# Performance work log

Hardware: AMD Instinct MI355X
Metric: run time of the kernel (lower is better)

Reference implementation:

```python
import jax, jax.numpy as jnp
import numpy as np

E = 16      # num experts
K = 2       # top-k
EPS = np.finfo(float).eps


def setup_inputs() -> dict:
    key = jax.random.key(0)
    k1, k2, k3 = jax.random.split(key, 3)
    B, D_IN, D_OUT = 16384, 1024, 512
    x = jax.random.normal(k1, (B, D_IN), dtype=jnp.float32)
    w_router = jax.random.normal(k2, (D_IN, E), dtype=jnp.float32) * 0.02
    w_experts = jax.random.normal(k3, (E, D_IN, D_OUT), dtype=jnp.float32) * 0.02
    return {"x": x, "w_router": w_router, "w_experts": w_experts}


def reference(x, w_router, w_experts):
    # --- noisy_top_k_gating (eval path: clean logits, no noise) ---
    logits = x @ w_router                      # [B, E]
    top_vals, top_idx = jax.lax.top_k(logits, K)   # [B, K]
    top_gates = jax.nn.softmax(top_vals, axis=1)   # softmax over top-k logits
    B = x.shape[0]
    gates = jnp.zeros_like(logits).at[jnp.arange(B)[:, None], top_idx].set(top_gates)  # [B, E]

    # --- per-expert encode (dense form; zero gates null out non-dispatched pairs,
    #     matching SparseDispatcher's sparse dispatch/combine math exactly) ---
    expert_out = jnp.einsum('bd,edh->beh', x, w_experts)  # [B, E, d_out]

    # --- SparseDispatcher.combine: exp -> gate-weight -> index_add -> eps clamp -> log ---
    combined = jnp.einsum('be,beh->bh', gates, jnp.exp(expert_out))  # [B, d_out]
    combined = jnp.where(combined == 0, jnp.asarray(EPS, combined.dtype), combined)
    return jnp.log(combined)
```

## Files before the change

### kernel.cpp

```cpp
#include <hip/hip_runtime.h>
#include <hip/hip_bf16.h>
#include <stdint.h>

typedef unsigned short u16_t;
typedef unsigned int   u32_t;

#define B_ROWS  16384
#define D_IN    1024
#define D_OUT   512
#define NEXP    16
#define CNT_STRIDE 16
#define EPSF    2.2204460492503131e-16f

using short8  = __attribute__((ext_vector_type(8))) short;
using floatx4 = __attribute__((ext_vector_type(4))) float;

__device__ __forceinline__ u16_t f2bf(float f) {
    u32_t u = __float_as_uint(f);
    u += 0x7fffu + ((u >> 16) & 1u);
    return (u16_t)(u >> 16);
}

__device__ __forceinline__ void gload_lds16(const void* g, void* l) {
    __builtin_amdgcn_global_load_lds(
        (const __attribute__((address_space(1))) void*)g,
        (__attribute__((address_space(3))) void*)l, 16, 0, 0);
}

__global__ __launch_bounds__(256) void prep_kernel(
        const float* __restrict__ wr, float* __restrict__ wrT,
        const float* __restrict__ we, u16_t* __restrict__ wT,
        int* __restrict__ counts) {
    int b = blockIdx.x, t = threadIdx.x;
    if (b < 64) {
        int i = b * 256 + t;
        int e = i >> 10, d = i & 1023;
        wrT[i] = wr[d * NEXP + e];
    } else if (b == 64) {
        counts[t] = 0;
    } else {
        int bb = b - 65;
        int e  = bb >> 8;
        int k0 = ((bb >> 1) & 127) * 8;
        int n  = (bb & 1) * 256 + t;
        const float* src = we + ((size_t)e * D_IN + k0) * D_OUT + n;
        union { u16_t us[8]; uint4 v; } p;
        #pragma unroll
        for (int j = 0; j < 8; ++j) p.us[j] = f2bf(src[(size_t)j * D_OUT]);
        *(uint4*)(wT + ((size_t)e * D_OUT + n) * D_IN + k0) = p.v;
    }
}

__global__ __launch_bounds__(256) void router_kernel(
        const float* __restrict__ x, const float* __restrict__ wrT,
        int* __restrict__ counts, int* __restrict__ rowlist,
        float* __restrict__ gatelist, u16_t* __restrict__ xb) {
    __shared__ float wsh[NEXP * D_IN];
    __shared__ int hist[NEXP], base[NEXP], hist2[NEXP];
    __shared__ unsigned char eidx_sh[32][2];
    __shared__ float g_sh[32][2];

    int t = threadIdx.x;
    {
        const float4* src = (const float4*)wrT;
        float4* dst = (float4*)wsh;
        #pragma unroll
        for (int i = 0; i < 16; ++i) dst[t + 256 * i] = src[t + 256 * i];
    }
    if (t < NEXP) { hist[t] = 0; hist2[t] = 0; }
    __syncthreads();

    int lr = t >> 3, c = t & 7;
    int row = blockIdx.x * 32 + lr;
    const float4* xr = (const float4*)(x + (size_t)row * D_IN);

    double acc[NEXP];
    #pragma unroll
    for (int e = 0; e < NEXP; ++e) acc[e] = 0.0;

    for (int i = 0; i < 32; ++i) {
        int f4 = i * 8 + c;
        float4 xv = xr[f4];
        int d = f4 * 4;
        if (xb) {
            uint2 pk;
            pk.x = (u32_t)f2bf(xv.x) | ((u32_t)f2bf(xv.y) << 16);
            pk.y = (u32_t)f2bf(xv.z) | ((u32_t)f2bf(xv.w) << 16);
            *(uint2*)(xb + (size_t)row * D_IN + d) = pk;
        }
        double x0 = xv.x, x1 = xv.y, x2 = xv.z, x3 = xv.w;
        #pragma unroll
        for (int e = 0; e < NEXP; ++e) {
            float4 wv = *(const float4*)(&wsh[e * D_IN + d]);
            acc[e] += x0 * (double)wv.x;
            acc[e] += x1 * (double)wv.y;
            acc[e] += x2 * (double)wv.z;
            acc[e] += x3 * (double)wv.w;
        }
    }
    #pragma unroll
    for (int e = 0; e < NEXP; ++e) {
        acc[e] += __shfl_xor(acc[e], 1);
        acc[e] += __shfl_xor(acc[e], 2);
        acc[e] += __shfl_xor(acc[e], 4);
    }
    if (c == 0) {
        int i1 = 0; double v1 = acc[0];
        #pragma unroll
        for (int e = 1; e < NEXP; ++e) if (acc[e] > v1) { v1 = acc[e]; i1 = e; }
        int i2 = -1; double v2 = -1.0e300;
        #pragma unroll
        for (int e = 0; e < NEXP; ++e) if (e != i1 && acc[e] > v2) { v2 = acc[e]; i2 = e; }
        double ed = exp(v2 - v1);
        double s = 1.0 + ed;
        eidx_sh[lr][0] = (unsigned char)i1; g_sh[lr][0] = (float)(1.0 / s);
        eidx_sh[lr][1] = (unsigned char)i2; g_sh[lr][1] = (float)(ed / s);
        atomicAdd(&hist[i1], 1);
        atomicAdd(&hist[i2], 1);
    }
    __syncthreads();
    if (t < NEXP) base[t] = atomicAdd(&counts[t * CNT_STRIDE], hist[t]);
    __syncthreads();
    if (t < 64) {
        int r = t >> 1, sl = t & 1;
        int e = eidx_sh[r][sl];
        int pos = base[e] + atomicAdd(&hist2[e], 1);
        rowlist[e * B_ROWS + pos] = ((blockIdx.x * 32 + r) << 1) | sl;
        gatelist[e * B_ROWS + pos] = g_sh[r][sl];
    }
}

template<bool USE_CONTRIB>
__global__ __launch_bounds__(256) void moe_gemm_bf16(
        const u16_t* __restrict__ xb, const u16_t* __restrict__ wT,
        const int* __restrict__ counts, const int* __restrict__ rowlist,
        const float* __restrict__ gatelist,
        float* __restrict__ out, float* __restrict__ contrib) {
    int bid = blockIdx.x;
    int s   = bid >> 3;
    int e   = ((bid & 7) << 1) | (s >> 9);
    s &= 511;
    int tx = s & 3, ty = s >> 2;
    int n_e = counts[e * CNT_STRIDE];
    if (ty * 128 >= n_e) return;
    int n0 = tx * 128;

    __shared__ u16_t Ash[128 * 64];
    __shared__ u16_t Bsh[128 * 64];
    __shared__ int   rid_sh[128];
    __shared__ float gt_sh[128];

    int t = threadIdx.x;
    if (t < 128) {
        int gi = ty * 128 + t;
        int v = 0; float g = 0.f;
        if (gi < n_e) { v = rowlist[e * B_ROWS + gi]; g = gatelist[e * B_ROWS + gi]; }
        rid_sh[t] = v; gt_sh[t] = g;
    }
    __syncthreads();

    int lane = t & 63, wv = t >> 6;

    const u16_t* asrc[4];
    const u16_t* bsrc[4];
    #pragma unroll
    for (int r = 0; r < 4; ++r) {
        int i   = r * 256 + wv * 64 + lane;
        int row = i >> 3;
        int ss  = (i & 7) ^ (row & 7);
        asrc[r] = xb + (size_t)(rid_sh[row] >> 1) * D_IN + ss * 8;
        bsrc[r] = wT + ((size_t)e * D_OUT + n0 + row) * D_IN + ss * 8;
    }

    int wm = wv >> 1, wn = wv & 1;
    int lm = lane & 15, q = lane >> 4;
    int l7 = lm & 7;

    floatx4 acc[4][4];
    #pragma unroll
    for (int mi = 0; mi < 4; ++mi)
        #pragma unroll
        for (int ni = 0; ni < 4; ++ni)
            acc[mi][ni] = (floatx4){0.f, 0.f, 0.f, 0.f};

    for (int it = 0; it < D_IN / 64; ++it) {
        if (it) __syncthreads();
        #pragma unroll
        for (int r = 0; r < 4; ++r) {
            gload_lds16(asrc[r], (char*)Ash + r * 4096 + wv * 1024);
            gload_lds16(bsrc[r], (char*)Bsh + r * 4096 + wv * 1024);
            asrc[r] += 64; bsrc[r] += 64;
        }
        __syncthreads();

        #pragma unroll
        for (int kk = 0; kk < 2; ++kk) {
            int sw = ((((kk << 2) | q) ^ l7) << 3);
            short8 afr[4], bfr[4];
            #pragma unroll
            for (int f = 0; f < 4; ++f) {
                afr[f] = *(const short8*)(Ash + ((wm * 64 + f * 16 + lm) << 6) + sw);
                bfr[f] = *(const short8*)(Bsh + ((wn * 64 + f * 16 + lm) << 6) + sw);
            }
            #pragma unroll
            for (int mi = 0; mi < 4; ++mi)
                #pragma unroll
                for (int ni = 0; ni < 4; ++ni)
                    acc[mi][ni] = __builtin_amdgcn_mfma_f32_16x16x32_bf16(
                        afr[mi], bfr[ni], acc[mi][ni], 0, 0, 0);
        }
    }

    #pragma unroll
    for (int mi = 0; mi < 4; ++mi) {
        int rbase = wm * 64 + mi * 16 + q * 4;
        #pragma unroll
        for (int r = 0; r < 4; ++r) {
            int row = rbase + r;
            int gi = ty * 128 + row;
            bool ok = gi < n_e;
            int v = rid_sh[row];
            float g = gt_sh[row];
            size_t orow = (size_t)(v >> 1) * D_OUT;
            #pragma unroll
            for (int ni = 0; ni < 4; ++ni) {
                int c = n0 + wn * 64 + ni * 16 + lm;
                float val = g * __expf(acc[mi][ni][r]);
                if (ok) {
                    if (USE_CONTRIB) {
                        float* dst = (v & 1) ? contrib : out;
                        dst[orow + c] = val;
                    } else {
                        atomicAdd(&out[orow + c], val);
                    }
                }
            }
        }
    }
}

template<bool USE_CONTRIB>
__global__ __launch_bounds__(256) void moe_gemm(
        const float* __restrict__ x, const float* __restrict__ w,
        const int* __restrict__ counts, const int* __restrict__ rowlist,
        const float* __restrict__ gatelist,
        float* __restrict__ out, float* __restrict__ contrib) {
    int e = blockIdx.z;
    int n_e = counts[e * CNT_STRIDE];
    int ty = blockIdx.y;
    if (ty * 128 >= n_e) return;
    int n0 = blockIdx.x * 128;

    __shared__ u16_t Ash[128][40];
    __shared__ u32_t Bsh[16][132];
    __shared__ int   rid_sh[128];
    __shared__ float gt_sh[128];

    int t = threadIdx.x;
    if (t < 128) {
        int gi = ty * 128 + t;
        int v = 0; float g = 0.f;
        if (gi < n_e) { v = rowlist[e * B_ROWS + gi]; g = gatelist[e * B_ROWS + gi]; }
        rid_sh[t] = v; gt_sh[t] = g;
    }
    __syncthreads();

    int ar = t >> 1, ah = t & 1;
    const float* xptr = x + (size_t)(rid_sh[ar] >> 1) * D_IN + ah * 16;
    int bkp = t >> 4, bng = t & 15;
    const float* wptr = w + (size_t)e * (D_IN * D_OUT)
                          + (size_t)(2 * bkp) * D_OUT + n0 + bng * 8;

    int lane = t & 63, wv = t >> 6;
    int wm = wv >> 1, wn = wv & 1;
    int lm = lane & 15, q = lane >> 4;

    floatx4 acc[4][4];
    #pragma unroll
    for (int mi = 0; mi < 4; ++mi)
        #pragma unroll
        for (int ni = 0; ni < 4; ++ni)
            acc[mi][ni] = (floatx4){0.f, 0.f, 0.f, 0.f};

    for (int it = 0; it < D_IN / 32; ++it) {
        float4 av0 = *(const float4*)(xptr + 0);
        float4 av1 = *(const float4*)(xptr + 4);
        float4 av2 = *(const float4*)(xptr + 8);
        float4 av3 = *(const float4*)(xptr + 12);
        xptr += 32;
        float4 b0 = *(const float4*)(wptr + 0);
        float4 b1 = *(const float4*)(wptr + 4);
        float4 b2 = *(const float4*)(wptr + D_OUT);
        float4 b3 = *(const float4*)(wptr + D_OUT + 4);
        wptr += 32 * D_OUT;

        __syncthreads();
        {
            union { u16_t us[16]; uint4 v[2]; } ap;
            float af[16] = {av0.x, av0.y, av0.z, av0.w, av1.x, av1.y, av1.z, av1.w,
                            av2.x, av2.y, av2.z, av2.w, av3.x, av3.y, av3.z, av3.w};
            #pragma unroll
            for (int j = 0; j < 16; ++j) ap.us[j] = f2bf(af[j]);
            *(uint4*)(&Ash[ar][ah * 16])     = ap.v[0];
            *(uint4*)(&Ash[ar][ah * 16 + 8]) = ap.v[1];
        }
        {
            union { u32_t up[8]; uint4 v[2]; } bp;
            bp.up[0] = (u32_t)f2bf(b0.x) | ((u32_t)f2bf(b2.x) << 16);
            bp.up[1] = (u32_t)f2bf(b0.y) | ((u32_t)f2bf(b2.y) << 16);
            bp.up[2] = (u32_t)f2bf(b0.z) | ((u32_t)f2bf(b2.z) << 16);
            bp.up[3] = (u32_t)f2bf(b0.w) | ((u32_t)f2bf(b2.w) << 16);
            bp.up[4] = (u32_t)f2bf(b1.x) | ((u32_t)f2bf(b3.x) << 16);
            bp.up[5] = (u32_t)f2bf(b1.y) | ((u32_t)f2bf(b3.y) << 16);
            bp.up[6] = (u32_t)f2bf(b1.z) | ((u32_t)f2bf(b3.z) << 16);
            bp.up[7] = (u32_t)f2bf(b1.w) | ((u32_t)f2bf(b3.w) << 16);
            *(uint4*)(&Bsh[bkp][bng * 8])     = bp.v[0];
            *(uint4*)(&Bsh[bkp][bng * 8 + 4]) = bp.v[1];
        }
        __syncthreads();

        short8 afr[4];
        #pragma unroll
        for (int mi = 0; mi < 4; ++mi)
            afr[mi] = *(const short8*)(&Ash[wm * 64 + mi * 16 + lm][q * 8]);
        short8 bfr[4];
        #pragma unroll
        for (int ni = 0; ni < 4; ++ni) {
            int nn = wn * 64 + ni * 16 + lm;
            union { uint4 u; short8 s; } cv;
            cv.u.x = Bsh[q * 4 + 0][nn];
            cv.u.y = Bsh[q * 4 + 1][nn];
            cv.u.z = Bsh[q * 4 + 2][nn];
            cv.u.w = Bsh[q * 4 + 3][nn];
            bfr[ni] = cv.s;
        }
        #pragma unroll
        for (int mi = 0; mi < 4; ++mi)
            #pragma unroll
            for (int ni = 0; ni < 4; ++ni)
                acc[mi][ni] = __builtin_amdgcn_mfma_f32_16x16x32_bf16(
                    afr[mi], bfr[ni], acc[mi][ni], 0, 0, 0);
    }

    #pragma unroll
    for (int mi = 0; mi < 4; ++mi) {
        int rbase = wm * 64 + mi * 16 + q * 4;
        #pragma unroll
        for (int r = 0; r < 4; ++r) {
            int row = rbase + r;
            int gi = ty * 128 + row;
            bool ok = gi < n_e;
            int v = rid_sh[row];
            float g = gt_sh[row];
            size_t orow = (size_t)(v >> 1) * D_OUT;
            #pragma unroll
            for (int ni = 0; ni < 4; ++ni) {
                int c = n0 + wn * 64 + ni * 16 + lm;
                float val = g * __expf(acc[mi][ni][r]);
                if (ok) {
                    if (USE_CONTRIB) {
                        float* dst = (v & 1) ? contrib : out;
                        dst[orow + c] = val;
                    } else {
                        atomicAdd(&out[orow + c], val);
                    }
                }
            }
        }
    }
}

__global__ __launch_bounds__(256) void combine_add_log(
        float* __restrict__ out, const float* __restrict__ contrib, int n4) {
    int i = blockIdx.x * blockDim.x + threadIdx.x;
    if (i >= n4) return;
    float4 a = ((const float4*)out)[i];
    float4 b = ((const float4*)contrib)[i];
    float4 r;
    float s;
    s = a.x + b.x; s = (s == 0.f) ? EPSF : s; r.x = __logf(s);
    s = a.y + b.y; s = (s == 0.f) ? EPSF : s; r.y = __logf(s);
    s = a.z + b.z; s = (s == 0.f) ? EPSF : s; r.z = __logf(s);
    s = a.w + b.w; s = (s == 0.f) ? EPSF : s; r.w = __logf(s);
    ((float4*)out)[i] = r;
}

__global__ __launch_bounds__(256) void log_inplace(float* __restrict__ out, int n4) {
    int i = blockIdx.x * blockDim.x + threadIdx.x;
    if (i >= n4) return;
    float4 a = ((float4*)out)[i];
    float4 r;
    float s;
    s = a.x; s = (s == 0.f) ? EPSF : s; r.x = __logf(s);
    s = a.y; s = (s == 0.f) ? EPSF : s; r.y = __logf(s);
    s = a.z; s = (s == 0.f) ? EPSF : s; r.z = __logf(s);
    s = a.w; s = (s == 0.f) ? EPSF : s; r.w = __logf(s);
    ((float4*)out)[i] = r;
}

extern "C" void kernel_launch(void* const* d_in, const int* in_sizes, int n_in,
                              void* d_out, int out_size, void* d_ws, size_t ws_size,
                              hipStream_t stream) {
    const float* x  = (const float*)d_in[0];
    const float* wr = (const float*)d_in[1];
    const float* we = (const float*)d_in[2];
    float* out = (float*)d_out;
    char* ws = (char*)d_ws;

    size_t off = 0;
    int*   counts  = (int*)(ws + off);   off += 1024;
    int*   rowlist = (int*)(ws + off);   off += (size_t)NEXP * B_ROWS * 4;
    float* gates   = (float*)(ws + off); off += (size_t)NEXP * B_ROWS * 4;
    float* wrT     = (float*)(ws + off); off += (size_t)NEXP * D_IN * 4;
    float* contrib = (float*)(ws + off); off += (size_t)B_ROWS * D_OUT * 4;
    size_t tier2_need = off;
    u16_t* xb      = (u16_t*)(ws + off); off += (size_t)B_ROWS * D_IN * 2;
    u16_t* wTb     = (u16_t*)(ws + off); off += (size_t)NEXP * D_IN * D_OUT * 2;
    size_t tier3_need = off;

    bool tier3 = ws_size >= tier3_need;
    bool tier2 = ws_size >= tier2_need;

    prep_kernel<<<tier3 ? (65 + NEXP * 256) : 65, 256, 0, stream>>>(
        wr, wrT, we, wTb, counts);
    router_kernel<<<B_ROWS / 32, 256, 0, stream>>>(
        x, wrT, counts, rowlist, gates, tier3 ? xb : (u16_t*)nullptr);

    int n4 = B_ROWS * D_OUT / 4;

    if (tier3) {
        moe_gemm_bf16<true><<<8192, 256, 0, stream>>>(
            xb, wTb, counts, rowlist, gates, out, contrib);
        combine_add_log<<<(n4 + 255) / 256, 256, 0, stream>>>(out, contrib, n4);
    } else if (tier2) {
        dim3 g(D_OUT / 128, B_ROWS / 128, NEXP);
        moe_gemm<true><<<g, 256, 0, stream>>>(x, we, counts, rowlist, gates, out, contrib);
        combine_add_log<<<(n4 + 255) / 256, 256, 0, stream>>>(out, contrib, n4);
    } else {
        dim3 g(D_OUT / 128, B_ROWS / 128, NEXP);
        hipMemsetAsync(out, 0, (size_t)B_ROWS * D_OUT * 4, stream);
        moe_gemm<false><<<g, 256, 0, stream>>>(x, we, counts, rowlist, gates, out, nullptr);
        log_inplace<<<(n4 + 255) / 256, 256, 0, stream>>>(out, n4);
    }
}
```

Baseline: 240.6 us.

## Restructure router to drop LDS weight staging and read router weights from cache

The router kernel no longer copies the 64KB transposed router weight matrix into shared memory per block. It reads the weights directly from global memory, relying on L1/L2 caching. Each row is now handled by 32 lanes instead of 8, with 16 rows per 512-thread block, and all x loads are issued up front. This removes the per-block LDS fill and the occupancy limit that the large shared array imposed. In exchange it adds two more shuffle-reduction stages and more global/cache traffic for the weights.

```diff
diff --git a/kernel.cpp b/kernel.cpp
--- a/kernel.cpp
+++ b/kernel.cpp
@@ -51,47 +51,49 @@
     }
 }
 
-__global__ __launch_bounds__(256) void router_kernel(
+__global__ __launch_bounds__(512) void router_kernel(
         const float* __restrict__ x, const float* __restrict__ wrT,
         int* __restrict__ counts, int* __restrict__ rowlist,
         float* __restrict__ gatelist, u16_t* __restrict__ xb) {
-    __shared__ float wsh[NEXP * D_IN];
     __shared__ int hist[NEXP], base[NEXP], hist2[NEXP];
-    __shared__ unsigned char eidx_sh[32][2];
-    __shared__ float g_sh[32][2];
+    __shared__ unsigned char eidx_sh[16][2];
+    __shared__ float g_sh[16][2];
 
     int t = threadIdx.x;
-    {
-        const float4* src = (const float4*)wrT;
-        float4* dst = (float4*)wsh;
-        #pragma unroll
-        for (int i = 0; i < 16; ++i) dst[t + 256 * i] = src[t + 256 * i];
-    }
     if (t < NEXP) { hist[t] = 0; hist2[t] = 0; }
     __syncthreads();
 
-    int lr = t >> 3, c = t & 7;
-    int row = blockIdx.x * 32 + lr;
-    const float4* xr = (const float4*)(x + (size_t)row * D_IN);
+    int lr = t >> 5, c = t & 31;
+    int row = blockIdx.x * 16 + lr;
+    const float* xr = x + (size_t)row * D_IN + c * 4;
+    const float4* wr4 = (const float4*)wrT;
+
+    float4 xv[8];
+    #pragma unroll
+    for (int i = 0; i < 8; ++i)
+        xv[i] = *(const float4*)(xr + i * 128);
+
+    if (xb) {
+        #pragma unroll
+        for (int i = 0; i < 8; ++i) {
+            uint2 pk;
+            pk.x = (u32_t)f2bf(xv[i].x) | ((u32_t)f2bf(xv[i].y) << 16);
+            pk.y = (u32_t)f2bf(xv[i].z) | ((u32_t)f2bf(xv[i].w) << 16);
+            *(uint2*)(xb + (size_t)row * D_IN + c * 4 + i * 128) = pk;
+        }
+    }
 
     double acc[NEXP];
     #pragma unroll
     for (int e = 0; e < NEXP; ++e) acc[e] = 0.0;
 
-    for (int i = 0; i < 32; ++i) {
-        int f4 = i * 8 + c;
-        float4 xv = xr[f4];
-        int d = f4 * 4;
-        if (xb) {
-            uint2 pk;
-            pk.x = (u32_t)f2bf(xv.x) | ((u32_t)f2bf(xv.y) << 16);
-            pk.y = (u32_t)f2bf(xv.z) | ((u32_t)f2bf(xv.w) << 16);
-            *(uint2*)(xb + (size_t)row * D_IN + d) = pk;
-        }
-        double x0 = xv.x, x1 = xv.y, x2 = xv.z, x3 = xv.w;
+    #pragma unroll
+    for (int i = 0; i < 8; ++i) {
+        int f4 = c + i * 32;
+        double x0 = xv[i].x, x1 = xv[i].y, x2 = xv[i].z, x3 = xv[i].w;
         #pragma unroll
         for (int e = 0; e < NEXP; ++e) {
-            float4 wv = *(const float4*)(&wsh[e * D_IN + d]);
+            float4 wv = wr4[e * 256 + f4];
             acc[e] += x0 * (double)wv.x;
             acc[e] += x1 * (double)wv.y;
             acc[e] += x2 * (double)wv.z;
@@ -103,6 +105,8 @@
         acc[e] += __shfl_xor(acc[e], 1);
         acc[e] += __shfl_xor(acc[e], 2);
         acc[e] += __shfl_xor(acc[e], 4);
+        acc[e] += __shfl_xor(acc[e], 8);
+        acc[e] += __shfl_xor(acc[e], 16);
     }
     if (c == 0) {
         int i1 = 0; double v1 = acc[0];
@@ -121,11 +125,11 @@
     __syncthreads();
     if (t < NEXP) base[t] = atomicAdd(&counts[t * CNT_STRIDE], hist[t]);
     __syncthreads();
-    if (t < 64) {
+    if (t < 32) {
         int r = t >> 1, sl = t & 1;
         int e = eidx_sh[r][sl];
         int pos = base[e] + atomicAdd(&hist2[e], 1);
-        rowlist[e * B_ROWS + pos] = ((blockIdx.x * 32 + r) << 1) | sl;
+        rowlist[e * B_ROWS + pos] = ((blockIdx.x * 16 + r) << 1) | sl;
         gatelist[e * B_ROWS + pos] = g_sh[r][sl];
     }
 }
@@ -423,7 +427,7 @@
 
     prep_kernel<<<tier3 ? (65 + NEXP * 256) : 65, 256, 0, stream>>>(
         wr, wrT, we, wTb, counts);
-    router_kernel<<<B_ROWS / 32, 256, 0, stream>>>(
+    router_kernel<<<B_ROWS / 16, 512, 0, stream>>>(
         x, wrT, counts, rowlist, gates, tier3 ? xb : (u16_t*)nullptr);
 
     int n4 = B_ROWS * D_OUT / 4;
```

After: 284.9 us. 1.18x slower.
